# Kernel optimization log

Hardware: AMD Instinct MI355X
Metric: run time of the kernel (lower is better)

Reference implementation:

```python
import jax, jax.numpy as jnp
import numpy as np

SEQ, BATCH, IN_DIM, HID_DIM = 512, 256, 256, 256
NQ = 8
ALPHA = 0.5
MLP_HID = 128


def _linear_init(key, fan_in, fan_out):
    k1, k2 = jax.random.split(key)
    bound = 1.0 / np.sqrt(fan_in)
    W = jax.random.uniform(k1, (fan_in, fan_out), minval=-bound, maxval=bound, dtype=jnp.float32)
    b = jax.random.uniform(k2, (fan_out,), minval=-bound, maxval=bound, dtype=jnp.float32)
    return W, b


def setup_inputs() -> dict:
    key = jax.random.key(0)
    ks = jax.random.split(key, 12)
    cdim = IN_DIM + HID_DIM
    inputs = jax.random.normal(ks[0], (SEQ, BATCH, IN_DIM), dtype=jnp.float32)
    W1, b1 = _linear_init(ks[1], cdim, MLP_HID)
    W2, b2 = _linear_init(ks[2], MLP_HID, NQ * 4)
    Wf, bf = _linear_init(ks[3], cdim, 1)
    Wi, bi = _linear_init(ks[4], cdim, 1)
    Wg, bg = _linear_init(ks[5], cdim, 1)
    Wo, bo = _linear_init(ks[6], cdim, 1)
    rzf = jax.random.normal(ks[7], (NQ,), dtype=jnp.float32)
    rzi = jax.random.normal(ks[8], (NQ,), dtype=jnp.float32)
    rzg = jax.random.normal(ks[9], (NQ,), dtype=jnp.float32)
    rzo = jax.random.normal(ks[10], (NQ,), dtype=jnp.float32)
    return dict(inputs=inputs, W1=W1, b1=b1, W2=W2, b2=b2,
                Wf=Wf, bf=bf, Wi=Wi, bi=bi, Wg=Wg, bg=bg, Wo=Wo, bo=bo,
                rzf=rzf, rzi=rzi, rzg=rzg, rzo=rzo)


def _qgate(theta):
    # Analytic expectations of the RX/RZ/CNOT-chain circuit:
    # <Z_k> = prod_{j<=k} cos(theta_j); rz_params cancel in Z expectations.
    # Returns mean over wires, shape (batch, 1).
    return jnp.mean(jnp.cumprod(jnp.cos(theta), axis=-1), axis=-1, keepdims=True)


def reference(inputs, W1, b1, W2, b2, Wf, bf, Wi, bi, Wg, bg, Wo, bo, rzf, rzi, rzg, rzo):
    batch = inputs.shape[1]
    hx0 = jnp.zeros((batch, HID_DIM), dtype=inputs.dtype)
    cx0 = jnp.zeros((batch, HID_DIM), dtype=inputs.dtype)

    def step(carry, x):
        hx, cx = carry
        combined = jnp.concatenate([x, hx], axis=1)  # (B, in+hid)
        f_c = jax.nn.sigmoid(combined @ Wf + bf)
        i_c = jax.nn.sigmoid(combined @ Wi + bi)
        g_c = jnp.tanh(combined @ Wg + bg)
        o_c = jax.nn.sigmoid(combined @ Wo + bo)
        h1 = jax.nn.relu(combined @ W1 + b1)
        q = h1 @ W2 + b2  # (B, 4*NQ)
        q_f = _qgate(q[:, 0 * NQ:1 * NQ])
        q_i = _qgate(q[:, 1 * NQ:2 * NQ])
        q_g = _qgate(q[:, 2 * NQ:3 * NQ])
        q_o = _qgate(q[:, 3 * NQ:4 * NQ])
        f = (1 - ALPHA) * f_c + ALPHA * jax.nn.sigmoid(q_f)
        i = (1 - ALPHA) * i_c + ALPHA * jax.nn.sigmoid(q_i)
        g = (1 - ALPHA) * g_c + ALPHA * jnp.tanh(q_g)
        o = (1 - ALPHA) * o_c + ALPHA * jax.nn.sigmoid(q_o)
        cx_new = f * cx + i * g
        hx_new = o * jnp.tanh(cx_new)
        return (hx_new, cx_new), hx_new

    (hx, cx), outputs = jax.lax.scan(step, (hx0, cx0), inputs)
    return outputs, (hx, cx)
```

## Files before the change

### kernel.cpp

```cpp
#include <hip/hip_runtime.h>

#define SEQ 512
#define BATCH 256
#define INDIM 256
#define MLP 128
#define M_ROWS (SEQ * BATCH)
#define PRE_STRIDE 136
#define AUX_OFF ((size_t)M_ROWS * PRE_STRIDE)


__global__ __launch_bounds__(256) void prep_kernel(
    const float* __restrict__ W1,
    const float* __restrict__ Wf, const float* __restrict__ Wi,
    const float* __restrict__ Wg, const float* __restrict__ Wo,
    const float* __restrict__ bf, const float* __restrict__ bi,
    const float* __restrict__ bg, const float* __restrict__ bo,
    float* __restrict__ aux) {
  const int tid = threadIdx.x;
  if (tid < 128) {
    float s = 0.f;
    for (int k = 0; k < 256; ++k) s += W1[(size_t)(256 + k) * 128 + tid];
    aux[tid] = s;
  } else if (tid < 132) {
    const int g = tid - 128;
    const float* w = (g == 0) ? Wf : (g == 1) ? Wi : (g == 2) ? Wg : Wo;
    float s = 0.f;
    for (int k = 0; k < 256; ++k) s += w[256 + k];
    aux[128 + g] = s;
  } else if (tid < 136) {
    const int g = tid - 132;
    const float* bp = (g == 0) ? bf : (g == 1) ? bi : (g == 2) ? bg : bo;
    aux[132 + g] = bp[0];
  }
}

#define BK 16
#define LDX 132

__global__ __attribute__((amdgpu_waves_per_eu(1, 3))) __launch_bounds__(256)
void gemm_kernel(
    const float* __restrict__ X,
    const float* __restrict__ W1,
    const float* __restrict__ b1p,
    const float* __restrict__ Wf, const float* __restrict__ Wi,
    const float* __restrict__ Wg, const float* __restrict__ Wo,
    const float* __restrict__ bfp, const float* __restrict__ bip,
    const float* __restrict__ bgp, const float* __restrict__ bop,
    float* __restrict__ PRE) {
  __shared__ __align__(16) float Xs[BK * LDX];
  __shared__ __align__(16) float Ws[BK * LDX];
  __shared__ float Wgs[BK * 4];

  const int tid = threadIdx.x;
  const int blk = blockIdx.x;
  const int tx = tid & 15, ty = tid >> 4;
  const int r_st = tid >> 1, kh = (tid & 1) * 8;
  const int wk = tid >> 4, wn = (tid & 15) * 8;
  const int r2 = tid >> 1, gp = (tid & 1) * 2;

  const size_t rowbase = (size_t)blk * 128;

  float acc[8][8] = {};
  float ga = 0.f, gb = 0.f;

  float4 xa = *(const float4*)&X[(rowbase + r_st) * 256 + 0 + kh];
  float4 xb = *(const float4*)&X[(rowbase + r_st) * 256 + 0 + kh + 4];
  float4 wa = *(const float4*)&W1[(size_t)(0 + wk) * 128 + wn];
  float4 wb = *(const float4*)&W1[(size_t)(0 + wk) * 128 + wn + 4];
  float wgv = 0.f;
  if (tid < 64) {
    const int kk = tid >> 2, g = tid & 3;
    const float* w = (g == 0) ? Wf : (g == 1) ? Wi : (g == 2) ? Wg : Wo;
    wgv = w[0 + kk];
  }

  for (int kc = 0; kc < 256; kc += BK) {
    __syncthreads();
    Xs[(kh + 0) * LDX + r_st] = xa.x;
    Xs[(kh + 1) * LDX + r_st] = xa.y;
    Xs[(kh + 2) * LDX + r_st] = xa.z;
    Xs[(kh + 3) * LDX + r_st] = xa.w;
    Xs[(kh + 4) * LDX + r_st] = xb.x;
    Xs[(kh + 5) * LDX + r_st] = xb.y;
    Xs[(kh + 6) * LDX + r_st] = xb.z;
    Xs[(kh + 7) * LDX + r_st] = xb.w;
    *(float4*)&Ws[wk * LDX + wn] = wa;
    *(float4*)&Ws[wk * LDX + wn + 4] = wb;
    if (tid < 64) Wgs[tid] = wgv;
    __syncthreads();

    if (kc + BK < 256) {
      const int kn = kc + BK;
      xa = *(const float4*)&X[(rowbase + r_st) * 256 + kn + kh];
      xb = *(const float4*)&X[(rowbase + r_st) * 256 + kn + kh + 4];
      wa = *(const float4*)&W1[(size_t)(kn + wk) * 128 + wn];
      wb = *(const float4*)&W1[(size_t)(kn + wk) * 128 + wn + 4];
      if (tid < 64) {
        const int kk = tid >> 2, g = tid & 3;
        const float* w = (g == 0) ? Wf : (g == 1) ? Wi : (g == 2) ? Wg : Wo;
        wgv = w[kn + kk];
      }
    }

#pragma unroll
    for (int kk = 0; kk < BK; ++kk) {
      const float4 a0 = *(const float4*)&Xs[kk * LDX + ty * 8];
      const float4 a1 = *(const float4*)&Xs[kk * LDX + ty * 8 + 4];
      const float4 c0 = *(const float4*)&Ws[kk * LDX + tx * 8];
      const float4 c1 = *(const float4*)&Ws[kk * LDX + tx * 8 + 4];
      const float av[8] = {a0.x, a0.y, a0.z, a0.w, a1.x, a1.y, a1.z, a1.w};
      const float bv[8] = {c0.x, c0.y, c0.z, c0.w, c1.x, c1.y, c1.z, c1.w};
#pragma unroll
      for (int i = 0; i < 8; ++i)
#pragma unroll
        for (int j = 0; j < 8; ++j)
          acc[i][j] = fmaf(av[i], bv[j], acc[i][j]);
      const float xv = Xs[kk * LDX + r2];
      ga = fmaf(xv, Wgs[kk * 4 + gp], ga);
      gb = fmaf(xv, Wgs[kk * 4 + gp + 1], gb);
    }
  }

  float bias[8];
  {
    const float4 u0 = *(const float4*)&b1p[tx * 8];
    const float4 u1 = *(const float4*)&b1p[tx * 8 + 4];
    bias[0] = u0.x; bias[1] = u0.y; bias[2] = u0.z; bias[3] = u0.w;
    bias[4] = u1.x; bias[5] = u1.y; bias[6] = u1.z; bias[7] = u1.w;
  }
#pragma unroll
  for (int i = 0; i < 8; ++i) {
    const size_t row = rowbase + ty * 8 + i;
    float4 o0, o1;
    o0.x = acc[i][0] + bias[0]; o0.y = acc[i][1] + bias[1];
    o0.z = acc[i][2] + bias[2]; o0.w = acc[i][3] + bias[3];
    o1.x = acc[i][4] + bias[4]; o1.y = acc[i][5] + bias[5];
    o1.z = acc[i][6] + bias[6]; o1.w = acc[i][7] + bias[7];
    *(float4*)&PRE[row * PRE_STRIDE + tx * 8] = o0;
    *(float4*)&PRE[row * PRE_STRIDE + tx * 8 + 4] = o1;
  }
  {
    const float ab = (gp == 0) ? bfp[0] : bgp[0];
    const float bb2 = (gp == 0) ? bip[0] : bop[0];
    float2 og;
    og.x = ga + ab; og.y = gb + bb2;
    *(float2*)&PRE[(rowbase + r2) * PRE_STRIDE + 128 + gp] = og;
  }
}

__device__ __forceinline__ float sigmoid_f(float x) {
  return __fdividef(1.0f, 1.0f + __expf(-x));
}
__device__ __forceinline__ float tanh_f(float x) {
  const float e = __expf(-2.0f * x);
  return __fdividef(1.0f - e, 1.0f + e);
}
__device__ __forceinline__ float readlane_f(float v, int lane) {
  return __int_as_float(__builtin_amdgcn_readlane(__float_as_int(v), lane));
}

__global__ __attribute__((amdgpu_waves_per_eu(1, 1))) __launch_bounds__(64)
void rec_kernel(
    const float* __restrict__ PRE, const float* __restrict__ W2,
    const float* __restrict__ b2, const float* __restrict__ aux,
    float* __restrict__ out) {
  __shared__ __align__(16) float h1s[128];

  const int l = threadIdx.x;
  const int b = blockIdx.x;
  const int m = l & 31, half = l >> 5;
  const int g = m >> 3;
  const int g8 = g * 8;

  float w2r[64];
#pragma unroll
  for (int u = 0; u < 64; ++u) w2r[u] = W2[(size_t)(half * 64 + u) * 32 + m];
  const float b2m = b2[m];
  const float2 s1 = *(const float2*)&aux[2 * l];
  const float4 sg = *(const float4*)&aux[128];

  float h = 0.f, c = 0.f;

  const float* pr0 = PRE + (size_t)b * PRE_STRIDE;
  const size_t ts = (size_t)BATCH * PRE_STRIDE;

  float2 p0 = *(const float2*)(pr0 + 0 * ts + 2 * l);
  float4 g0 = *(const float4*)(pr0 + 0 * ts + 128);
  float2 p1 = *(const float2*)(pr0 + 1 * ts + 2 * l);
  float4 g1 = *(const float4*)(pr0 + 1 * ts + 128);

  const float4* h1p = (const float4*)&h1s[half * 64];

  for (int t = 0; t < SEQ; ++t) {
    const float h10 = fmaxf(fmaf(h, s1.x, p0.x), 0.f);
    const float h11 = fmaxf(fmaf(h, s1.y, p0.y), 0.f);

    ((float2*)h1s)[l] = make_float2(h10, h11);
    asm volatile("" ::: "memory");

    const float zf = fmaf(h, sg.x, g0.x);
    const float zi = fmaf(h, sg.y, g0.y);
    const float zg = fmaf(h, sg.z, g0.z);
    const float zo = fmaf(h, sg.w, g0.w);
    const float cf = sigmoid_f(zf);
    const float ci = sigmoid_f(zi);
    const float cg = tanh_f(zg);
    const float co = sigmoid_f(zo);
    p0 = p1; g0 = g1;
    const int tn = (t + 2 < SEQ) ? (t + 2) : (SEQ - 1);
    p1 = *(const float2*)(pr0 + (size_t)tn * ts + 2 * l);
    g1 = *(const float4*)(pr0 + (size_t)tn * ts + 128);

    float q0 = 0.f, q1 = 0.f, q2 = 0.f, q3 = 0.f;
#pragma unroll
    for (int jj = 0; jj < 16; ++jj) {
      const float4 hv = h1p[jj];
      q0 = fmaf(hv.x, w2r[4 * jj + 0], q0);
      q1 = fmaf(hv.y, w2r[4 * jj + 1], q1);
      q2 = fmaf(hv.z, w2r[4 * jj + 2], q2);
      q3 = fmaf(hv.w, w2r[4 * jj + 3], q3);
    }
    const float part = (q0 + q1) + (q2 + q3);

    const float full = part + __shfl_xor(part, 32, 64);
    const float cm = __cosf(full + b2m);
    const int sb = (l & 32) + g8;
    const float e0 = __shfl(cm, sb + 0, 64);
    const float e1 = __shfl(cm, sb + 1, 64);
    const float e2 = __shfl(cm, sb + 2, 64);
    const float e3 = __shfl(cm, sb + 3, 64);
    const float e4 = __shfl(cm, sb + 4, 64);
    const float e5 = __shfl(cm, sb + 5, 64);
    const float e6 = __shfl(cm, sb + 6, 64);
    const float e7 = __shfl(cm, sb + 7, 64);
    float p = e0, s = e0;
    p *= e1; s += p;
    p *= e2; s += p;
    p *= e3; s += p;
    p *= e4; s += p;
    p *= e5; s += p;
    p *= e6; s += p;
    p *= e7; s += p;
    const float qv = s * 0.125f;

    const float qarg = (g == 2) ? (2.0f * qv) : qv;
    const float qs = sigmoid_f(qarg);
    const float av = (g == 2) ? (2.0f * qs - 1.0f) : qs;

    const float aF = readlane_f(av, 0);
    const float aI = readlane_f(av, 8);
    const float aG = readlane_f(av, 16);
    const float aO = readlane_f(av, 24);

    const float f  = 0.5f * (cf + aF);
    const float ii = 0.5f * (ci + aI);
    const float gg = 0.5f * (cg + aG);
    const float oo = 0.5f * (co + aO);

    c = fmaf(f, c, ii * gg);
    h = oo * tanh_f(c);

    float4 hv4o; hv4o.x = h; hv4o.y = h; hv4o.z = h; hv4o.w = h;
    *(float4*)(out + ((size_t)t * BATCH + b) * 256 + 4 * l) = hv4o;
  }

  float4 hq; hq.x = h; hq.y = h; hq.z = h; hq.w = h;
  float4 cq; cq.x = c; cq.y = c; cq.z = c; cq.w = c;
  *(float4*)(out + (size_t)SEQ * BATCH * 256 + (size_t)b * 256 + 4 * l) = hq;
  *(float4*)(out + (size_t)SEQ * BATCH * 256 + (size_t)BATCH * 256 +
             (size_t)b * 256 + 4 * l) = cq;
}

extern "C" void kernel_launch(void* const* d_in, const int* in_sizes, int n_in,
                              void* d_out, int out_size, void* d_ws,
                              size_t ws_size, hipStream_t stream) {
  const float* X  = (const float*)d_in[0];
  const float* W1 = (const float*)d_in[1];
  const float* b1 = (const float*)d_in[2];
  const float* W2 = (const float*)d_in[3];
  const float* b2 = (const float*)d_in[4];
  const float* Wf = (const float*)d_in[5];
  const float* bf = (const float*)d_in[6];
  const float* Wi = (const float*)d_in[7];
  const float* bi = (const float*)d_in[8];
  const float* Wg = (const float*)d_in[9];
  const float* bg = (const float*)d_in[10];
  const float* Wo = (const float*)d_in[11];
  const float* bo = (const float*)d_in[12];

  float* ws  = (float*)d_ws;
  float* PRE = ws;
  float* aux = ws + AUX_OFF;
  float* out = (float*)d_out;

  prep_kernel<<<1, 256, 0, stream>>>(W1, Wf, Wi, Wg, Wo, bf, bi, bg, bo, aux);
  gemm_kernel<<<M_ROWS / 128, 256, 0, stream>>>(X, W1, b1, Wf, Wi, Wg, Wo,
                                                bf, bi, bg, bo, PRE);
  rec_kernel<<<BATCH, 64, 0, stream>>>(PRE, W2, b2, aux, out);
}
```

Baseline: 767.1 us.

## Move input-projection GEMM to bf16x3 MFMA with pre-split transposed weights

Replaces the FP32 SIMT GEMM that computes the x-part of the MLP and gate pre-activations with MFMA 16x16x32 bf16 instructions. Each operand is split into high and low bf16 parts and three products are summed to keep near-fp32 accuracy. The prep kernel now transposes and splits the weights (W1 plus the four gate vectors, padded to 144 columns) into the workspace. The aim is to cut the compute time of the large GEMM. In exchange there are extra conversion work, more LDS traffic, and a serial single-block prep that grows.

```diff
diff --git a/kernel.cpp b/kernel.cpp
--- a/kernel.cpp
+++ b/kernel.cpp
@@ -8,6 +8,21 @@
 #define PRE_STRIDE 136
 #define AUX_OFF ((size_t)M_ROWS * PRE_STRIDE)
 
+#define BT_OFF (AUX_OFF + 160)
+
+typedef __attribute__((ext_vector_type(8))) short short8v;
+typedef __attribute__((ext_vector_type(4))) float f32x4;
+
+__device__ __forceinline__ unsigned short bf16_rtne(float f) {
+  unsigned u = __float_as_uint(f);
+  unsigned r = u + 0x7FFFu + ((u >> 16) & 1u);
+  return (unsigned short)(r >> 16);
+}
+__device__ __forceinline__ void cvt2(float f, unsigned short& h,
+                                     unsigned short& l) {
+  h = bf16_rtne(f);
+  l = bf16_rtne(f - __uint_as_float((unsigned)h << 16));
+}
 
 __global__ __launch_bounds__(256) void prep_kernel(
     const float* __restrict__ W1,
@@ -15,7 +30,8 @@
     const float* __restrict__ Wg, const float* __restrict__ Wo,
     const float* __restrict__ bf, const float* __restrict__ bi,
     const float* __restrict__ bg, const float* __restrict__ bo,
-    float* __restrict__ aux) {
+    const float* __restrict__ b1, float* __restrict__ aux,
+    float* __restrict__ btbase) {
   const int tid = threadIdx.x;
   if (tid < 128) {
     float s = 0.f;
@@ -32,119 +48,123 @@
     const float* bp = (g == 0) ? bf : (g == 1) ? bi : (g == 2) ? bg : bo;
     aux[132 + g] = bp[0];
   }
-}
-
-#define BK 16
-#define LDX 132
+
+  unsigned short* bth = (unsigned short*)btbase;
+  unsigned short* btl = (unsigned short*)(btbase + 18432);
+  float* b144 = btbase + 36864;
+  for (int tau = tid; tau < 576; tau += 256) {
+    const int n = tau >> 2, q = tau & 3;
+    const float* wg = (n == 129) ? Wi : (n == 130) ? Wg : (n == 131) ? Wo : Wf;
+    for (int k = q * 64; k < q * 64 + 64; ++k) {
+      const float v = (n < 128) ? W1[(size_t)k * 128 + n]
+                                : ((n < 132) ? wg[k] : 0.f);
+      unsigned short h, l;
+      cvt2(v, h, l);
+      bth[n * 256 + k] = h;
+      btl[n * 256 + k] = l;
+    }
+  }
+  if (tid < 144) {
+    const float bv = (tid < 128) ? b1[tid]
+                   : (tid == 128) ? bf[0] : (tid == 129) ? bi[0]
+                   : (tid == 130) ? bg[0] : (tid == 131) ? bo[0] : 0.f;
+    b144[tid] = bv;
+  }
+}
 
 __global__ __attribute__((amdgpu_waves_per_eu(1, 3))) __launch_bounds__(256)
-void gemm_kernel(
-    const float* __restrict__ X,
-    const float* __restrict__ W1,
-    const float* __restrict__ b1p,
-    const float* __restrict__ Wf, const float* __restrict__ Wi,
-    const float* __restrict__ Wg, const float* __restrict__ Wo,
-    const float* __restrict__ bfp, const float* __restrict__ bip,
-    const float* __restrict__ bgp, const float* __restrict__ bop,
-    float* __restrict__ PRE) {
-  __shared__ __align__(16) float Xs[BK * LDX];
-  __shared__ __align__(16) float Ws[BK * LDX];
-  __shared__ float Wgs[BK * 4];
+void gemm_kernel(const float* __restrict__ X,
+                 const unsigned short* __restrict__ Bth,
+                 const unsigned short* __restrict__ Btl,
+                 const float* __restrict__ bias144,
+                 float* __restrict__ PRE) {
+  __shared__ __align__(16) unsigned short Ah[4096];
+  __shared__ __align__(16) unsigned short Al[4096];
+  __shared__ __align__(16) unsigned short Bh[4608];
+  __shared__ __align__(16) unsigned short Bl[4608];
 
   const int tid = threadIdx.x;
-  const int blk = blockIdx.x;
-  const int tx = tid & 15, ty = tid >> 4;
-  const int r_st = tid >> 1, kh = (tid & 1) * 8;
-  const int wk = tid >> 4, wn = (tid & 15) * 8;
-  const int r2 = tid >> 1, gp = (tid & 1) * 2;
-
-  const size_t rowbase = (size_t)blk * 128;
-
-  float acc[8][8] = {};
-  float ga = 0.f, gb = 0.f;
-
-  float4 xa = *(const float4*)&X[(rowbase + r_st) * 256 + 0 + kh];
-  float4 xb = *(const float4*)&X[(rowbase + r_st) * 256 + 0 + kh + 4];
-  float4 wa = *(const float4*)&W1[(size_t)(0 + wk) * 128 + wn];
-  float4 wb = *(const float4*)&W1[(size_t)(0 + wk) * 128 + wn + 4];
-  float wgv = 0.f;
-  if (tid < 64) {
-    const int kk = tid >> 2, g = tid & 3;
-    const float* w = (g == 0) ? Wf : (g == 1) ? Wi : (g == 2) ? Wg : Wo;
-    wgv = w[0 + kk];
-  }
-
-  for (int kc = 0; kc < 256; kc += BK) {
+  const size_t rowbase = (size_t)blockIdx.x * 128;
+  const int lane = tid & 63, wv = tid >> 6;
+  const int l15 = lane & 15, kgl = lane >> 4;
+  const int mt0 = wv * 2, mt1 = wv * 2 + 1;
+
+  f32x4 acc0[9], acc1[9];
+#pragma unroll
+  for (int nt = 0; nt < 9; ++nt) {
+    acc0[nt] = (f32x4){0.f, 0.f, 0.f, 0.f};
+    acc1[nt] = (f32x4){0.f, 0.f, 0.f, 0.f};
+  }
+
+  for (int kc = 0; kc < 256; kc += 32) {
     __syncthreads();
-    Xs[(kh + 0) * LDX + r_st] = xa.x;
-    Xs[(kh + 1) * LDX + r_st] = xa.y;
-    Xs[(kh + 2) * LDX + r_st] = xa.z;
-    Xs[(kh + 3) * LDX + r_st] = xa.w;
-    Xs[(kh + 4) * LDX + r_st] = xb.x;
-    Xs[(kh + 5) * LDX + r_st] = xb.y;
-    Xs[(kh + 6) * LDX + r_st] = xb.z;
-    Xs[(kh + 7) * LDX + r_st] = xb.w;
-    *(float4*)&Ws[wk * LDX + wn] = wa;
-    *(float4*)&Ws[wk * LDX + wn + 4] = wb;
-    if (tid < 64) Wgs[tid] = wgv;
+#pragma unroll
+    for (int s = 0; s < 2; ++s) {
+      const int tau = tid + s * 256;
+      const int r = tau >> 2, kg = tau & 3;
+      const float4 xa = *(const float4*)&X[(rowbase + r) * 256 + kc + kg * 8];
+      const float4 xb =
+          *(const float4*)&X[(rowbase + r) * 256 + kc + kg * 8 + 4];
+      unsigned short h0, h1, h2, h3, h4, h5, h6, h7;
+      unsigned short l0, l1, l2, l3, l4, l5, l6, l7;
+      cvt2(xa.x, h0, l0); cvt2(xa.y, h1, l1);
+      cvt2(xa.z, h2, l2); cvt2(xa.w, h3, l3);
+      cvt2(xb.x, h4, l4); cvt2(xb.y, h5, l5);
+      cvt2(xb.z, h6, l6); cvt2(xb.w, h7, l7);
+      const short8v hv = {(short)h0, (short)h1, (short)h2, (short)h3,
+                          (short)h4, (short)h5, (short)h6, (short)h7};
+      const short8v lv = {(short)l0, (short)l1, (short)l2, (short)l3,
+                          (short)l4, (short)l5, (short)l6, (short)l7};
+      const int dst = (((r >> 4) * 4 + kg) * 16 + (r & 15)) * 8;
+      *(short8v*)&Ah[dst] = hv;
+      *(short8v*)&Al[dst] = lv;
+    }
+#pragma unroll
+    for (int s = 0; s < 3; ++s) {
+      const int tau = tid + s * 256;
+      if (tau < 576) {
+        const int n = tau >> 2, kg = tau & 3;
+        const int src = n * 256 + kc + kg * 8;
+        const int dst = (((n >> 4) * 4 + kg) * 16 + (n & 15)) * 8;
+        *(short8v*)&Bh[dst] = *(const short8v*)&Bth[src];
+        *(short8v*)&Bl[dst] = *(const short8v*)&Btl[src];
+      }
+    }
     __syncthreads();
 
-    if (kc + BK < 256) {
-      const int kn = kc + BK;
-      xa = *(const float4*)&X[(rowbase + r_st) * 256 + kn + kh];
-      xb = *(const float4*)&X[(rowbase + r_st) * 256 + kn + kh + 4];
-      wa = *(const float4*)&W1[(size_t)(kn + wk) * 128 + wn];
-      wb = *(const float4*)&W1[(size_t)(kn + wk) * 128 + wn + 4];
-      if (tid < 64) {
-        const int kk = tid >> 2, g = tid & 3;
-        const float* w = (g == 0) ? Wf : (g == 1) ? Wi : (g == 2) ? Wg : Wo;
-        wgv = w[kn + kk];
+    const int ab0 = ((mt0 * 4 + kgl) * 16 + l15) * 8;
+    const int ab1 = ((mt1 * 4 + kgl) * 16 + l15) * 8;
+    const short8v ah0 = *(const short8v*)&Ah[ab0];
+    const short8v al0 = *(const short8v*)&Al[ab0];
+    const short8v ah1 = *(const short8v*)&Ah[ab1];
+    const short8v al1 = *(const short8v*)&Al[ab1];
+#pragma unroll
+    for (int nt = 0; nt < 9; ++nt) {
+      const int bb = ((nt * 4 + kgl) * 16 + l15) * 8;
+      const short8v bh = *(const short8v*)&Bh[bb];
+      const short8v bl = *(const short8v*)&Bl[bb];
+      acc0[nt] = __builtin_amdgcn_mfma_f32_16x16x32_bf16(ah0, bh, acc0[nt], 0, 0, 0);
+      acc0[nt] = __builtin_amdgcn_mfma_f32_16x16x32_bf16(ah0, bl, acc0[nt], 0, 0, 0);
+      acc0[nt] = __builtin_amdgcn_mfma_f32_16x16x32_bf16(al0, bh, acc0[nt], 0, 0, 0);
+      acc1[nt] = __builtin_amdgcn_mfma_f32_16x16x32_bf16(ah1, bh, acc1[nt], 0, 0, 0);
+      acc1[nt] = __builtin_amdgcn_mfma_f32_16x16x32_bf16(ah1, bl, acc1[nt], 0, 0, 0);
+      acc1[nt] = __builtin_amdgcn_mfma_f32_16x16x32_bf16(al1, bh, acc1[nt], 0, 0, 0);
+    }
+  }
+
+#pragma unroll
+  for (int nt = 0; nt < 9; ++nt) {
+    const int col = nt * 16 + l15;
+    if (col < 132) {
+      const float bb = bias144[col];
+#pragma unroll
+      for (int q = 0; q < 4; ++q) {
+        PRE[(rowbase + mt0 * 16 + kgl * 4 + q) * PRE_STRIDE + col] =
+            acc0[nt][q] + bb;
+        PRE[(rowbase + mt1 * 16 + kgl * 4 + q) * PRE_STRIDE + col] =
+            acc1[nt][q] + bb;
       }
     }
-
-#pragma unroll
-    for (int kk = 0; kk < BK; ++kk) {
-      const float4 a0 = *(const float4*)&Xs[kk * LDX + ty * 8];
-      const float4 a1 = *(const float4*)&Xs[kk * LDX + ty * 8 + 4];
-      const float4 c0 = *(const float4*)&Ws[kk * LDX + tx * 8];
-      const float4 c1 = *(const float4*)&Ws[kk * LDX + tx * 8 + 4];
-      const float av[8] = {a0.x, a0.y, a0.z, a0.w, a1.x, a1.y, a1.z, a1.w};
-      const float bv[8] = {c0.x, c0.y, c0.z, c0.w, c1.x, c1.y, c1.z, c1.w};
-#pragma unroll
-      for (int i = 0; i < 8; ++i)
-#pragma unroll
-        for (int j = 0; j < 8; ++j)
-          acc[i][j] = fmaf(av[i], bv[j], acc[i][j]);
-      const float xv = Xs[kk * LDX + r2];
-      ga = fmaf(xv, Wgs[kk * 4 + gp], ga);
-      gb = fmaf(xv, Wgs[kk * 4 + gp + 1], gb);
-    }
-  }
-
-  float bias[8];
-  {
-    const float4 u0 = *(const float4*)&b1p[tx * 8];
-    const float4 u1 = *(const float4*)&b1p[tx * 8 + 4];
-    bias[0] = u0.x; bias[1] = u0.y; bias[2] = u0.z; bias[3] = u0.w;
-    bias[4] = u1.x; bias[5] = u1.y; bias[6] = u1.z; bias[7] = u1.w;
-  }
-#pragma unroll
-  for (int i = 0; i < 8; ++i) {
-    const size_t row = rowbase + ty * 8 + i;
-    float4 o0, o1;
-    o0.x = acc[i][0] + bias[0]; o0.y = acc[i][1] + bias[1];
-    o0.z = acc[i][2] + bias[2]; o0.w = acc[i][3] + bias[3];
-    o1.x = acc[i][4] + bias[4]; o1.y = acc[i][5] + bias[5];
-    o1.z = acc[i][6] + bias[6]; o1.w = acc[i][7] + bias[7];
-    *(float4*)&PRE[row * PRE_STRIDE + tx * 8] = o0;
-    *(float4*)&PRE[row * PRE_STRIDE + tx * 8 + 4] = o1;
-  }
-  {
-    const float ab = (gp == 0) ? bfp[0] : bgp[0];
-    const float bb2 = (gp == 0) ? bip[0] : bop[0];
-    float2 og;
-    og.x = ga + ab; og.y = gb + bb2;
-    *(float2*)&PRE[(rowbase + r2) * PRE_STRIDE + 128 + gp] = og;
   }
 }
 
@@ -291,10 +311,14 @@
   float* ws  = (float*)d_ws;
   float* PRE = ws;
   float* aux = ws + AUX_OFF;
+  float* btbase = ws + BT_OFF;
+  const unsigned short* bth = (const unsigned short*)btbase;
+  const unsigned short* btl = (const unsigned short*)(btbase + 18432);
+  const float* b144 = btbase + 36864;
   float* out = (float*)d_out;
 
-  prep_kernel<<<1, 256, 0, stream>>>(W1, Wf, Wi, Wg, Wo, bf, bi, bg, bo, aux);
-  gemm_kernel<<<M_ROWS / 128, 256, 0, stream>>>(X, W1, b1, Wf, Wi, Wg, Wo,
-                                                bf, bi, bg, bo, PRE);
+  prep_kernel<<<1, 256, 0, stream>>>(W1, Wf, Wi, Wg, Wo, bf, bi, bg, bo,
+                                     b1, aux, btbase);
+  gemm_kernel<<<M_ROWS / 128, 256, 0, stream>>>(X, bth, btl, b144, PRE);
   rec_kernel<<<BATCH, 64, 0, stream>>>(PRE, W2, b2, aux, out);
 }
```

New measurement: 799.8 us. +4.3%, slower.
